# Kernel optimization log

Measured on AMD Instinct MI355X. Metric: run time of the kernel, lower is better.

## Reference

```python
import jax, jax.numpy as jnp
import numpy as np

D_MODEL = 1024
N_Q = 16
N_KV = 4
GRP = N_Q // N_KV
DQ = 64
DV = 64
B = 2
S = 2048
EPS = 1e-5


def _rope(x):
    # x: (N, S, ..., d) with sequence on axis 1; interleaved-pair rotary, theta=10000
    seq, d = x.shape[1], x.shape[-1]
    inv_freq = 1.0 / (10000.0 ** (jnp.arange(0, d, 2, dtype=jnp.float32) / d))
    ang = jnp.arange(seq, dtype=jnp.float32)[:, None] * inv_freq[None, :]  # (S, d/2)
    bshape = (1, seq) + (1,) * (x.ndim - 3) + (d // 2,)
    cos = jnp.cos(ang).reshape(bshape).astype(x.dtype)
    sin = jnp.sin(ang).reshape(bshape).astype(x.dtype)
    x1, x2 = x[..., 0::2], x[..., 1::2]
    r1 = x1 * cos - x2 * sin
    r2 = x1 * sin + x2 * cos
    return jnp.stack([r1, r2], axis=-1).reshape(x.shape)


def _layer_norm(x, gamma, beta):
    mu = jnp.mean(x, axis=-1, keepdims=True)
    var = jnp.var(x, axis=-1, keepdims=True)
    return (x - mu) * jax.lax.rsqrt(var + EPS) * gamma + beta


def setup_inputs() -> dict:
    key = jax.random.key(0)
    ks = jax.random.split(key, 13)
    scale = 0.02
    return {
        "query_sequences": jax.random.normal(ks[0], (B, S, D_MODEL), jnp.float32),
        "key_sequences": jax.random.normal(ks[1], (B, S, D_MODEL), jnp.float32),
        "value_sequences": jax.random.normal(ks[2], (B, S, D_MODEL), jnp.float32),
        "key_value_sequence_lengths": jax.random.randint(ks[3], (B,), S // 2, S + 1),
        "ln_gamma": jnp.ones((D_MODEL,), jnp.float32),
        "ln_beta": jnp.zeros((D_MODEL,), jnp.float32),
        "Wq": jax.random.normal(ks[4], (D_MODEL, N_Q * DQ), jnp.float32) * scale,
        "bq": jnp.zeros((N_Q * DQ,), jnp.float32),
        "Wk": jax.random.normal(ks[5], (D_MODEL, N_KV * DQ), jnp.float32) * scale,
        "bk": jnp.zeros((N_KV * DQ,), jnp.float32),
        "Wv": jax.random.normal(ks[6], (D_MODEL, N_KV * DV), jnp.float32) * scale,
        "bv": jnp.zeros((N_KV * DV,), jnp.float32),
        "Wo": jax.random.normal(ks[7], (N_Q * DV, D_MODEL), jnp.float32) * scale,
        "bo": jnp.zeros((D_MODEL,), jnp.float32),
    }


def reference(query_sequences, key_sequences, value_sequences,
              key_value_sequence_lengths, ln_gamma, ln_beta,
              Wq, bq, Wk, bk, Wv, bv, Wo, bo):
    N, t = query_sequences.shape[0], query_sequences.shape[1]
    T = key_sequences.shape[1]
    # pre-LN (self-attn: applied to q, k, v inputs)
    q_in = _layer_norm(query_sequences, ln_gamma, ln_beta)
    k_in = _layer_norm(key_sequences, ln_gamma, ln_beta)
    v_in = _layer_norm(value_sequences, ln_gamma, ln_beta)
    q = (q_in @ Wq + bq).reshape(N, t, N_KV, GRP, DQ)      # (N,t,h,H,d)
    k = (k_in @ Wk + bk).reshape(N, T, N_KV, DQ)           # (N,T,h,d)
    v = (v_in @ Wv + bv).reshape(N, T, N_KV, DV)           # (N,T,h,d)
    q = _rope(q)
    k = _rope(k)
    scores = jnp.einsum('nthHd,nThd->nhHtT', q, k) / jnp.sqrt(jnp.float32(DQ))
    key_pos = jnp.arange(T)
    pad_ok = (key_pos[None, :] < key_value_sequence_lengths[:, None])  # (N,T)
    causal_ok = (jnp.arange(t)[:, None] >= key_pos[None, :])           # (t,T)
    mask = pad_ok[:, None, None, None, :] & causal_ok[None, None, None, :, :]
    scores = jnp.where(mask, scores, -jnp.inf)
    attn = jax.nn.softmax(scores, axis=-1)                 # (N,h,H,t,T)
    attn_viz = jnp.transpose(attn, (0, 2, 1, 3, 4))        # (N,H,h,t,T)
    seq = jnp.einsum('nhHtT,nThd->nthHd', attn, v).reshape(N, t, N_Q * DV)
    out = seq @ Wo + bo
    return out, attn_viz
```

## Files before the change

### kernel.cpp

```cpp
#include <hip/hip_runtime.h>
#include <hip/hip_bf16.h>

#define S_LEN 2048
#define DM 1024

typedef __attribute__((ext_vector_type(8))) short s16x8;
typedef __attribute__((ext_vector_type(4))) float f32x4;
typedef __attribute__((ext_vector_type(4))) ushort u16x4;

__device__ __forceinline__ ushort f2bf(float f){
  union { float f; unsigned u; } v; v.f = f;
  unsigned r = (v.u + 0x7FFFu + ((v.u >> 16) & 1u)) >> 16;
  return (ushort)r;
}

__device__ __forceinline__ f32x4 mfma16(s16x8 a, s16x8 b, f32x4 c){
  return __builtin_amdgcn_mfma_f32_16x16x32_bf16(a, b, c, 0, 0, 0);
}

__device__ __forceinline__ void gl_lds16(const ushort* g, ushort* l){
  __builtin_amdgcn_global_load_lds(
      (const __attribute__((address_space(1))) unsigned int*)g,
      (__attribute__((address_space(3))) unsigned int*)l, 16, 0, 0);
}

__global__ __launch_bounds__(256) void trig_kernel(float* __restrict__ tab){
  int idx = blockIdx.x*256 + threadIdx.x;
  int t = idx >> 5, i2 = idx & 31;
  float inv = exp2f(-(float)i2 * 0.4152410118609203f);
  float ang = (float)t * inv;
  tab[2*idx]   = cosf(ang);
  tab[2*idx+1] = sinf(ang);
}

__global__ __launch_bounds__(256) void ln_kernel(const float* __restrict__ x,
    const float* __restrict__ g, const float* __restrict__ be, ushort* __restrict__ o){
  int row = blockIdx.x;
  int tid = threadIdx.x;
  const float* xr = x + (size_t)row*DM;
  float4 xv = *(const float4*)(xr + tid*4);
  float s  = xv.x+xv.y+xv.z+xv.w;
  float s2 = xv.x*xv.x+xv.y*xv.y+xv.z*xv.z+xv.w*xv.w;
  for (int m=1;m<64;m<<=1){ s += __shfl_xor(s,m); s2 += __shfl_xor(s2,m); }
  __shared__ float red[8];
  int w = tid>>6, l = tid&63;
  if (l==0){ red[w]=s; red[4+w]=s2; }
  __syncthreads();
  float ts = red[0]+red[1]+red[2]+red[3];
  float t2 = red[4]+red[5]+red[6]+red[7];
  float mu  = ts*(1.0f/DM);
  float var = t2*(1.0f/DM) - mu*mu;
  float rs  = rsqrtf(var + 1e-5f);
  float vals[4] = {xv.x,xv.y,xv.z,xv.w};
  const float* gp = g + tid*4;
  const float* bp = be + tid*4;
  u16x4 ov;
  #pragma unroll
  for (int j=0;j<4;j++) ov[j] = f2bf((vals[j]-mu)*rs*gp[j] + bp[j]);
  *(u16x4*)(o + (size_t)row*DM + tid*4) = ov;
}

__global__ __launch_bounds__(256) void wtr_kernel(const float* __restrict__ in,
    ushort* __restrict__ out, int N){
  __shared__ float lsf[32][36];
  int tid = threadIdx.x;
  int n0 = blockIdx.x*32, k0 = blockIdx.y*32;
  int kr = tid>>3, nc = (tid&7)*4;
  float4 v = *(const float4*)(in + (size_t)(k0+kr)*N + n0 + nc);
  *(float4*)&lsf[kr][nc] = v;
  __syncthreads();
  int nr = tid>>3, kc = (tid&7)*4;
  u16x4 o;
  #pragma unroll
  for (int j=0;j<4;j++) o[j] = f2bf(lsf[kc+j][nr]);
  *(u16x4*)(out + (size_t)(n0+nr)*DM + k0 + kc) = o;
}

__global__ __launch_bounds__(256) void utr_kernel(const ushort* __restrict__ vb,
    ushort* __restrict__ vt){
  __shared__ ushort lst[64*72];
  int tid = threadIdx.x;
  int t0 = blockIdx.x*64;
  int y = blockIdx.y; int n = y>>2, h = y&3;
  int Tr = tid>>2, dg = (tid&3)*16;
  const ushort* ip = vb + ((size_t)(n*S_LEN + t0 + Tr))*256 + h*64 + dg;
  *(s16x8*)&lst[Tr*72 + dg]     = *(const s16x8*)ip;
  *(s16x8*)&lst[Tr*72 + dg + 8] = *(const s16x8*)(ip+8);
  __syncthreads();
  int d = tid>>2, Tg = (tid&3)*16;
  ushort* op = vt + ((size_t)(y*64 + d))*S_LEN + t0 + Tg;
  #pragma unroll
  for (int q=0;q<4;q++){
    u16x4 o;
    #pragma unroll
    for (int j=0;j<4;j++) o[j] = lst[(Tg+4*q+j)*72 + d];
    *(u16x4*)(op + 4*q) = o;
  }
}

template<int BN, bool ROPE, bool F32OUT>
__global__ __launch_bounds__(256) void gemm_kernel(
    const ushort* __restrict__ A, const ushort* __restrict__ BT,
    const float* __restrict__ bias, const float* __restrict__ tab,
    void* __restrict__ Cv, int N, int K){
  constexpr int NB = BN/32;
  __shared__ ushort Als[128*32];
  __shared__ ushort Bls[BN*32];
  int tid = threadIdx.x;
  int w = tid>>6, l = tid&63, lg = l>>4, li = l&15;
  int wr = w>>1, wc = w&1;
  int mbase = blockIdx.y*128, nbase = blockIdx.x*BN;
  f32x4 acc[4][NB];
  #pragma unroll
  for (int m=0;m<4;m++)
    #pragma unroll
    for (int n=0;n<NB;n++) acc[m][n] = (f32x4){0.f,0.f,0.f,0.f};
  int cr = l>>2, ck = (l&3)*8;
  for (int kk=0; kk<K; kk+=32){
    __syncthreads();
    #pragma unroll
    for (int s=0;s<2;s++){
      int ch = w*2+s;
      gl_lds16(A + (size_t)(mbase + ch*16 + cr)*K + kk + ck, &Als[ch*512]);
    }
    #pragma unroll
    for (int s=0;s<BN/64;s++){
      int ch = w*(BN/64)+s;
      gl_lds16(BT + (size_t)(nbase + ch*16 + cr)*K + kk + ck, &Bls[ch*512]);
    }
    __syncthreads();
    s16x8 af[4], bf[NB];
    #pragma unroll
    for (int m=0;m<4;m++) af[m] = *(const s16x8*)&Als[(wr*64 + m*16 + li)*32 + lg*8];
    #pragma unroll
    for (int n=0;n<NB;n++) bf[n] = *(const s16x8*)&Bls[(wc*(BN/2) + n*16 + li)*32 + lg*8];
    #pragma unroll
    for (int m=0;m<4;m++)
      #pragma unroll
      for (int n=0;n<NB;n++)
        acc[m][n] = mfma16(af[m], bf[n], acc[m][n]);
  }
  #pragma unroll
  for (int n=0;n<NB;n++){
    int gcol = nbase + wc*(BN/2) + n*16 + li;
    float bv = bias[gcol];
    #pragma unroll
    for (int m=0;m<4;m++){
      #pragma unroll
      for (int r=0;r<4;r++){
        int grow = mbase + wr*64 + m*16 + 4*lg + r;
        float val = acc[m][n][r] + bv;
        if (ROPE){
          int t = grow & (S_LEN-1);
          int d = gcol & 63;
          const float* tp = tab + t*64 + (d & 62);
          float cv = tp[0], sv = tp[1];
          float other = __shfl_xor(val, 1);
          val = (d & 1) ? (other*sv + val*cv) : (val*cv - other*sv);
        }
        if (F32OUT) ((float*)Cv)[(size_t)grow*N + gcol] = val;
        else        ((ushort*)Cv)[(size_t)grow*N + gcol] = f2bf(val);
      }
    }
  }
}

__global__ __launch_bounds__(256) void flash_kernel(
    const ushort* __restrict__ qg, const ushort* __restrict__ kg,
    const ushort* __restrict__ vt, const int* __restrict__ lens,
    ushort* __restrict__ seq, float* __restrict__ mbuf, float* __restrict__ lbuf){
  __shared__ ushort kls[64*72];
  __shared__ ushort vls[64*72];
  __shared__ ushort pls[64*72];
  int tid = threadIdx.x;
  int w = tid>>6, l = tid&63, lg = l>>4, li = l&15;
  int qbase = blockIdx.x*64;
  int qh = blockIdx.y;
  int n  = blockIdx.z;
  int h = qh>>2;
  int len = lens[n];
  const float L2E = 1.4426950408889634f;

  int trow = qbase + 16*w + li;
  const ushort* qp = qg + ((size_t)n*S_LEN + trow)*1024 + qh*64 + 8*lg;
  s16x8 qf0 = *(const s16x8*)qp;
  s16x8 qf1 = *(const s16x8*)(qp + 32);

  int sT = tid>>2, sdg = (tid&3)*16;
  const ushort* kp = kg + ((size_t)n*S_LEN + sT)*256 + h*64 + sdg;
  const ushort* vp = vt + ((size_t)((n*4+h)*64 + sT))*S_LEN + sdg;

  float m_r[4], l_r[4];
  f32x4 oacc[4];
  #pragma unroll
  for (int r=0;r<4;r++){ m_r[r] = -1e30f; l_r[r] = 0.f; }
  #pragma unroll
  for (int c=0;c<4;c++) oacc[c] = (f32x4){0.f,0.f,0.f,0.f};
  int Tlim = min(qbase + 63, len - 1);
  int nComp = (Tlim >> 6) + 1;

  for (int it=0; it<nComp; ++it){
    int Tb = it*64;
    __syncthreads();
    { const ushort* kpp = kp + (size_t)Tb*256;
      *(s16x8*)&kls[sT*72 + sdg]     = *(const s16x8*)kpp;
      *(s16x8*)&kls[sT*72 + sdg + 8] = *(const s16x8*)(kpp + 8);
      const ushort* vpp = vp + Tb;
      *(s16x8*)&vls[sT*72 + sdg]     = *(const s16x8*)vpp;
      *(s16x8*)&vls[sT*72 + sdg + 8] = *(const s16x8*)(vpp + 8);
    }
    __syncthreads();
    f32x4 sc[4];
    #pragma unroll
    for (int c=0;c<4;c++) sc[c] = (f32x4){0.f,0.f,0.f,0.f};
    #pragma unroll
    for (int c=0;c<4;c++){
      s16x8 b0 = *(const s16x8*)&kls[(16*c+li)*72 + 8*lg];
      s16x8 b1 = *(const s16x8*)&kls[(16*c+li)*72 + 8*lg + 32];
      sc[c] = mfma16(qf0, b0, sc[c]);
      sc[c] = mfma16(qf1, b1, sc[c]);
    }
    #pragma unroll
    for (int c=0;c<4;c++){
      int Tg = Tb + 16*c + li;
      bool colp = Tg < len;
      #pragma unroll
      for (int r=0;r<4;r++){
        int tg = qbase + 16*w + 4*lg + r;
        sc[c][r] = (colp && Tg <= tg) ? sc[c][r]*0.125f : -1e30f;
      }
    }
    float sf[4];
    #pragma unroll
    for (int r=0;r<4;r++){
      float tmax = fmaxf(fmaxf(sc[0][r], sc[1][r]), fmaxf(sc[2][r], sc[3][r]));
      for (int msk=1; msk<16; msk<<=1) tmax = fmaxf(tmax, __shfl_xor(tmax, msk));
      float mn = fmaxf(m_r[r], tmax);
      #pragma unroll
      for (int c=0;c<4;c++) sc[c][r] = exp2f((sc[c][r]-mn)*L2E);
      float ssum = sc[0][r]+sc[1][r]+sc[2][r]+sc[3][r];
      for (int msk=1; msk<16; msk<<=1) ssum += __shfl_xor(ssum, msk);
      sf[r] = exp2f((m_r[r]-mn)*L2E);
      l_r[r] = l_r[r]*sf[r] + ssum;
      m_r[r] = mn;
    }
    #pragma unroll
    for (int c=0;c<4;c++)
      #pragma unroll
      for (int r=0;r<4;r++) oacc[c][r] *= sf[r];
    #pragma unroll
    for (int c=0;c<4;c++)
      #pragma unroll
      for (int r=0;r<4;r++)
        pls[(16*w + 4*lg + r)*72 + 16*c + li] = f2bf(sc[c][r]);
    #pragma unroll
    for (int f=0; f<2; f++){
      s16x8 pa = *(const s16x8*)&pls[(16*w + li)*72 + 8*lg + 32*f];
      #pragma unroll
      for (int c=0;c<4;c++){
        s16x8 vf = *(const s16x8*)&vls[(16*c+li)*72 + 8*lg + 32*f];
        oacc[c] = mfma16(pa, vf, oacc[c]);
      }
    }
  }

  float inv_l[4];
  #pragma unroll
  for (int r=0;r<4;r++) inv_l[r] = 1.0f / l_r[r];
  #pragma unroll
  for (int c=0;c<4;c++){
    #pragma unroll
    for (int r=0;r<4;r++){
      int tg = qbase + 16*w + 4*lg + r;
      seq[((size_t)n*S_LEN + tg)*1024 + qh*64 + 16*c + li] = f2bf(oacc[c][r]*inv_l[r]);
    }
  }
  int zi = n*16 + qh;
  if (li == 0){
    #pragma unroll
    for (int r=0;r<4;r++){
      int tg = qbase + 16*w + 4*lg + r;
      mbuf[(size_t)zi*S_LEN + tg] = m_r[r];
      lbuf[(size_t)zi*S_LEN + tg] = inv_l[r];
    }
  }
}

__global__ __launch_bounds__(256) void viz_kernel(
    const ushort* __restrict__ qg, const ushort* __restrict__ kg,
    const int* __restrict__ lens, const float* __restrict__ mbuf,
    const float* __restrict__ lbuf, float* __restrict__ viz){
  __shared__ ushort kls[64*72];
  __shared__ float pfs[64*72];
  int tid = threadIdx.x;
  int Tb = blockIdx.x*64;
  int qbase = blockIdx.y*64;
  int zi = blockIdx.z;
  int n = zi>>4, qh = zi&15;
  int h = qh>>2, H = qh&3;
  int len = lens[n];
  float* vizp = viz + (size_t)((n*4 + H)*4 + h) * S_LEN * S_LEN;

  if (Tb > qbase + 63 || Tb >= len){
    int row = qbase + (tid>>2);
    float* zp = vizp + (size_t)row*S_LEN + Tb + (tid&3)*16;
    f32x4 zv = (f32x4){0.f,0.f,0.f,0.f};
    #pragma unroll
    for (int u=0;u<4;u++) *(f32x4*)(zp + 4*u) = zv;
    return;
  }

  int w = tid>>6, l = tid&63, lg = l>>4, li = l&15;
  const float L2E = 1.4426950408889634f;
  int trow = qbase + 16*w + li;
  const ushort* qp = qg + ((size_t)n*S_LEN + trow)*1024 + qh*64 + 8*lg;
  s16x8 qf0 = *(const s16x8*)qp;
  s16x8 qf1 = *(const s16x8*)(qp + 32);
  int sT = tid>>2, sdg = (tid&3)*16;
  const ushort* kpp = kg + ((size_t)n*S_LEN + Tb + sT)*256 + h*64 + sdg;
  *(s16x8*)&kls[sT*72 + sdg]     = *(const s16x8*)kpp;
  *(s16x8*)&kls[sT*72 + sdg + 8] = *(const s16x8*)(kpp + 8);

  float m_r[4], il_r[4];
  #pragma unroll
  for (int r=0;r<4;r++){
    int tg = qbase + 16*w + 4*lg + r;
    m_r[r]  = mbuf[(size_t)zi*S_LEN + tg];
    il_r[r] = lbuf[(size_t)zi*S_LEN + tg];
  }
  __syncthreads();

  f32x4 sc[4];
  #pragma unroll
  for (int c=0;c<4;c++) sc[c] = (f32x4){0.f,0.f,0.f,0.f};
  #pragma unroll
  for (int c=0;c<4;c++){
    s16x8 b0 = *(const s16x8*)&kls[(16*c+li)*72 + 8*lg];
    s16x8 b1 = *(const s16x8*)&kls[(16*c+li)*72 + 8*lg + 32];
    sc[c] = mfma16(qf0, b0, sc[c]);
    sc[c] = mfma16(qf1, b1, sc[c]);
  }
  #pragma unroll
  for (int c=0;c<4;c++){
    int Tg = Tb + 16*c + li;
    bool colp = Tg < len;
    #pragma unroll
    for (int r=0;r<4;r++){
      int tg = qbase + 16*w + 4*lg + r;
      bool ok = colp && (Tg <= tg);
      float p = exp2f((sc[c][r]*0.125f - m_r[r])*L2E) * il_r[r];
      pfs[(16*w + 4*lg + r)*72 + 16*c + li] = ok ? p : 0.f;
    }
  }
  __syncthreads();
  int row = tid>>2, c4 = (tid&3)*4;
  float* op = vizp + (size_t)(qbase+row)*S_LEN + Tb + c4;
  #pragma unroll
  for (int u=0;u<4;u++)
    *(f32x4*)(op + 16*u) = *(f32x4*)&pfs[row*72 + c4 + 16*u];
}

extern "C" void kernel_launch(void* const* d_in, const int* in_sizes, int n_in,
                              void* d_out, int out_size, void* d_ws, size_t ws_size,
                              hipStream_t stream){
  const float* xq = (const float*)d_in[0];
  const float* xk = (const float*)d_in[1];
  const float* xv = (const float*)d_in[2];
  const int*  lens= (const int*)d_in[3];
  const float* g  = (const float*)d_in[4];
  const float* be = (const float*)d_in[5];
  const float* Wq = (const float*)d_in[6];
  const float* bq = (const float*)d_in[7];
  const float* Wk = (const float*)d_in[8];
  const float* bk = (const float*)d_in[9];
  const float* Wv = (const float*)d_in[10];
  const float* bv = (const float*)d_in[11];
  const float* Wo = (const float*)d_in[12];
  const float* bo = (const float*)d_in[13];

  ushort* ws  = (ushort*)d_ws;
  ushort* xnq = ws;
  ushort* xnk = ws + 4194304;
  ushort* xnv = ws + 8388608;
  ushort* qb  = ws + 12582912;
  ushort* kb  = ws + 16777216;
  ushort* vb  = ws + 17825792;
  ushort* vt  = ws + 18874368;
  ushort* WqT = ws + 19922944;
  ushort* WkT = ws + 20971520;
  ushort* WvT = ws + 21233664;
  ushort* WoT = ws + 21495808;
  float*  tab = (float*)(ws + 22544384);
  float*  mbuf= (float*)(ws + 22806528);
  float*  lbuf= (float*)(ws + 22937600);
  ushort* seqb = xnq;

  float* outp = (float*)d_out;
  float* vizp = outp + (size_t)4194304;

  trig_kernel<<<256,256,0,stream>>>(tab);
  ln_kernel<<<4096,256,0,stream>>>(xq, g, be, xnq);
  ln_kernel<<<4096,256,0,stream>>>(xk, g, be, xnk);
  ln_kernel<<<4096,256,0,stream>>>(xv, g, be, xnv);
  wtr_kernel<<<dim3(32,32),256,0,stream>>>(Wq, WqT, 1024);
  wtr_kernel<<<dim3( 8,32),256,0,stream>>>(Wk, WkT, 256);
  wtr_kernel<<<dim3( 8,32),256,0,stream>>>(Wv, WvT, 256);
  wtr_kernel<<<dim3(32,32),256,0,stream>>>(Wo, WoT, 1024);
  gemm_kernel<128,true ,false><<<dim3(8,32),256,0,stream>>>(xnq, WqT, bq, tab, qb, 1024, 1024);
  gemm_kernel< 64,true ,false><<<dim3(4,32),256,0,stream>>>(xnk, WkT, bk, tab, kb,  256, 1024);
  gemm_kernel< 64,false,false><<<dim3(4,32),256,0,stream>>>(xnv, WvT, bv, tab, vb,  256, 1024);
  utr_kernel<<<dim3(32,8),256,0,stream>>>(vb, vt);
  flash_kernel<<<dim3(32,16,2),256,0,stream>>>(qb, kb, vt, lens, seqb, mbuf, lbuf);
  viz_kernel<<<dim3(32,32,32),256,0,stream>>>(qb, kb, lens, mbuf, lbuf, vizp);
  gemm_kernel<128,false,true ><<<dim3(8,32),256,0,stream>>>(seqb, WoT, bo, tab, (void*)outp, 1024, 1024);
}
```

Measured before the change: 866.3 us.

## Merge K/V projections, retile GEMMs, widen flash key blocks, batch viz tiles

```diff
diff --git a/kernel.cpp b/kernel.cpp
--- a/kernel.cpp
+++ b/kernel.cpp
@@ -33,11 +33,13 @@
   tab[2*idx+1] = sinf(ang);
 }
 
-__global__ __launch_bounds__(256) void ln_kernel(const float* __restrict__ x,
+__global__ __launch_bounds__(256) void ln3_kernel(const float* __restrict__ x0,
+    const float* __restrict__ x1, const float* __restrict__ x2,
     const float* __restrict__ g, const float* __restrict__ be, ushort* __restrict__ o){
   int row = blockIdx.x;
   int tid = threadIdx.x;
-  const float* xr = x + (size_t)row*DM;
+  const float* xs = (blockIdx.y==0) ? x0 : (blockIdx.y==1) ? x1 : x2;
+  const float* xr = xs + (size_t)row*DM;
   float4 xv = *(const float4*)(xr + tid*4);
   float s  = xv.x+xv.y+xv.z+xv.w;
   float s2 = xv.x*xv.x+xv.y*xv.y+xv.z*xv.z+xv.w*xv.w;
@@ -57,7 +59,7 @@
   u16x4 ov;
   #pragma unroll
   for (int j=0;j<4;j++) ov[j] = f2bf((vals[j]-mu)*rs*gp[j] + bp[j]);
-  *(u16x4*)(o + (size_t)row*DM + tid*4) = ov;
+  *(u16x4*)(o + (size_t)blockIdx.y*4194304 + (size_t)row*DM + tid*4) = ov;
 }
 
 __global__ __launch_bounds__(256) void wtr_kernel(const float* __restrict__ in,
@@ -76,14 +78,14 @@
   *(u16x4*)(out + (size_t)(n0+nr)*DM + k0 + kc) = o;
 }
 
-__global__ __launch_bounds__(256) void utr_kernel(const ushort* __restrict__ vb,
+__global__ __launch_bounds__(256) void utr_kernel(const ushort* __restrict__ kvb,
     ushort* __restrict__ vt){
   __shared__ ushort lst[64*72];
   int tid = threadIdx.x;
   int t0 = blockIdx.x*64;
   int y = blockIdx.y; int n = y>>2, h = y&3;
   int Tr = tid>>2, dg = (tid&3)*16;
-  const ushort* ip = vb + ((size_t)(n*S_LEN + t0 + Tr))*256 + h*64 + dg;
+  const ushort* ip = kvb + ((size_t)(n*S_LEN + t0 + Tr))*512 + 256 + h*64 + dg;
   *(s16x8*)&lst[Tr*72 + dg]     = *(const s16x8*)ip;
   *(s16x8*)&lst[Tr*72 + dg + 8] = *(const s16x8*)(ip+8);
   __syncthreads();
@@ -98,59 +100,74 @@
   }
 }
 
-template<int BN, bool ROPE, bool F32OUT>
+template<int BM, int MODE>
 __global__ __launch_bounds__(256) void gemm_kernel(
-    const ushort* __restrict__ A, const ushort* __restrict__ BT,
-    const float* __restrict__ bias, const float* __restrict__ tab,
+    const ushort* __restrict__ A, const ushort* __restrict__ A2,
+    const ushort* __restrict__ BT, const float* __restrict__ bias,
+    const float* __restrict__ bias2, const float* __restrict__ tab,
     void* __restrict__ Cv, int N, int K){
-  constexpr int NB = BN/32;
-  __shared__ ushort Als[128*32];
-  __shared__ ushort Bls[BN*32];
+  constexpr int MF = 2;
+  constexpr int NF = (BM == 128) ? 4 : 2;
+  constexpr int ACALLS = BM/32;
+  __shared__ ushort Als[BM*64];
+  __shared__ ushort Bls[64*64];
   int tid = threadIdx.x;
   int w = tid>>6, l = tid&63, lg = l>>4, li = l&15;
-  int wr = w>>1, wc = w&1;
-  int mbase = blockIdx.y*128, nbase = blockIdx.x*BN;
-  f32x4 acc[4][NB];
-  #pragma unroll
-  for (int m=0;m<4;m++)
-    #pragma unroll
-    for (int n=0;n<NB;n++) acc[m][n] = (f32x4){0.f,0.f,0.f,0.f};
-  int cr = l>>2, ck = (l&3)*8;
-  for (int kk=0; kk<K; kk+=32){
-    __syncthreads();
+  int wrow = (BM==128) ? w*32 : (w>>1)*32;
+  int wcol = (BM==128) ? 0 : (w&1)*32;
+  int mbase = blockIdx.y*BM, nbase = blockIdx.x*64;
+  const ushort* Ause = A;
+  if (MODE==2 && nbase >= 256) Ause = A2;
+  f32x4 acc[MF][NF];
+  #pragma unroll
+  for (int m=0;m<MF;m++)
+    #pragma unroll
+    for (int n=0;n<NF;n++) acc[m][n] = (f32x4){0.f,0.f,0.f,0.f};
+  for (int kk=0; kk<K; kk+=64){
+    __syncthreads();
+    #pragma unroll
+    for (int s=0;s<ACALLS;s++){
+      int idx = s*256 + tid;
+      int row = idx>>3, ch = idx&7;
+      gl_lds16(Ause + (size_t)(mbase+row)*K + kk + 8*(ch ^ (row&7)),
+               &Als[(size_t)(s*256 + w*64)*8]);
+    }
     #pragma unroll
     for (int s=0;s<2;s++){
-      int ch = w*2+s;
-      gl_lds16(A + (size_t)(mbase + ch*16 + cr)*K + kk + ck, &Als[ch*512]);
-    }
-    #pragma unroll
-    for (int s=0;s<BN/64;s++){
-      int ch = w*(BN/64)+s;
-      gl_lds16(BT + (size_t)(nbase + ch*16 + cr)*K + kk + ck, &Bls[ch*512]);
-    }
-    __syncthreads();
-    s16x8 af[4], bf[NB];
-    #pragma unroll
-    for (int m=0;m<4;m++) af[m] = *(const s16x8*)&Als[(wr*64 + m*16 + li)*32 + lg*8];
-    #pragma unroll
-    for (int n=0;n<NB;n++) bf[n] = *(const s16x8*)&Bls[(wc*(BN/2) + n*16 + li)*32 + lg*8];
-    #pragma unroll
-    for (int m=0;m<4;m++)
-      #pragma unroll
-      for (int n=0;n<NB;n++)
-        acc[m][n] = mfma16(af[m], bf[n], acc[m][n]);
-  }
-  #pragma unroll
-  for (int n=0;n<NB;n++){
-    int gcol = nbase + wc*(BN/2) + n*16 + li;
-    float bv = bias[gcol];
-    #pragma unroll
-    for (int m=0;m<4;m++){
+      int idx = s*256 + tid;
+      int row = idx>>3, ch = idx&7;
+      gl_lds16(BT + (size_t)(nbase+row)*K + kk + 8*(ch ^ (row&7)),
+               &Bls[(size_t)(s*256 + w*64)*8]);
+    }
+    __syncthreads();
+    #pragma unroll
+    for (int f=0;f<2;f++){
+      s16x8 af[MF], bfv[NF];
+      #pragma unroll
+      for (int m=0;m<MF;m++)
+        af[m] = *(const s16x8*)&Als[(wrow+m*16+li)*64 + 8*((lg+4*f) ^ (li&7))];
+      #pragma unroll
+      for (int n=0;n<NF;n++)
+        bfv[n] = *(const s16x8*)&Bls[(wcol+n*16+li)*64 + 8*((lg+4*f) ^ (li&7))];
+      #pragma unroll
+      for (int m=0;m<MF;m++)
+        #pragma unroll
+        for (int n=0;n<NF;n++)
+          acc[m][n] = mfma16(af[m], bfv[n], acc[m][n]);
+    }
+  }
+  bool doRope = (MODE==1) || (MODE==2 && nbase < 256);
+  #pragma unroll
+  for (int n=0;n<NF;n++){
+    int gcol = nbase + wcol + n*16 + li;
+    float bv0 = (MODE==2 && nbase>=256) ? bias2[gcol-256] : bias[gcol];
+    #pragma unroll
+    for (int m=0;m<MF;m++){
       #pragma unroll
       for (int r=0;r<4;r++){
-        int grow = mbase + wr*64 + m*16 + 4*lg + r;
-        float val = acc[m][n][r] + bv;
-        if (ROPE){
+        int grow = mbase + wrow + m*16 + 4*lg + r;
+        float val = acc[m][n][r] + bv0;
+        if (doRope){
           int t = grow & (S_LEN-1);
           int d = gcol & 63;
           const float* tp = tab + t*64 + (d & 62);
@@ -158,20 +175,20 @@
           float other = __shfl_xor(val, 1);
           val = (d & 1) ? (other*sv + val*cv) : (val*cv - other*sv);
         }
-        if (F32OUT) ((float*)Cv)[(size_t)grow*N + gcol] = val;
-        else        ((ushort*)Cv)[(size_t)grow*N + gcol] = f2bf(val);
+        if (MODE==3) ((float*)Cv)[(size_t)grow*N + gcol] = val;
+        else         ((ushort*)Cv)[(size_t)grow*N + gcol] = f2bf(val);
       }
     }
   }
 }
 
 __global__ __launch_bounds__(256) void flash_kernel(
-    const ushort* __restrict__ qg, const ushort* __restrict__ kg,
+    const ushort* __restrict__ qg, const ushort* __restrict__ kvb,
     const ushort* __restrict__ vt, const int* __restrict__ lens,
     ushort* __restrict__ seq, float* __restrict__ mbuf, float* __restrict__ lbuf){
-  __shared__ ushort kls[64*72];
-  __shared__ ushort vls[64*72];
-  __shared__ ushort pls[64*72];
+  __shared__ ushort kls[128*72];
+  __shared__ ushort vls[64*136];
+  __shared__ ushort pls[64*136];
   int tid = threadIdx.x;
   int w = tid>>6, l = tid&63, lg = l>>4, li = l&15;
   int qbase = blockIdx.x*64;
@@ -186,9 +203,10 @@
   s16x8 qf0 = *(const s16x8*)qp;
   s16x8 qf1 = *(const s16x8*)(qp + 32);
 
-  int sT = tid>>2, sdg = (tid&3)*16;
-  const ushort* kp = kg + ((size_t)n*S_LEN + sT)*256 + h*64 + sdg;
-  const ushort* vp = vt + ((size_t)((n*4+h)*64 + sT))*S_LEN + sdg;
+  int sT2 = tid>>1, sd2 = (tid&1)*32;
+  int dv  = tid>>2, tc  = (tid&3)*32;
+  const ushort* kp = kvb + ((size_t)n*S_LEN + sT2)*512 + h*64 + sd2;
+  const ushort* vp = vt + ((size_t)((n*4+h)*64 + dv))*S_LEN + tc;
 
   float m_r[4], l_r[4];
   f32x4 oacc[4];
@@ -197,31 +215,35 @@
   #pragma unroll
   for (int c=0;c<4;c++) oacc[c] = (f32x4){0.f,0.f,0.f,0.f};
   int Tlim = min(qbase + 63, len - 1);
-  int nComp = (Tlim >> 6) + 1;
-
-  for (int it=0; it<nComp; ++it){
-    int Tb = it*64;
-    __syncthreads();
-    { const ushort* kpp = kp + (size_t)Tb*256;
-      *(s16x8*)&kls[sT*72 + sdg]     = *(const s16x8*)kpp;
-      *(s16x8*)&kls[sT*72 + sdg + 8] = *(const s16x8*)(kpp + 8);
+  int nR = (Tlim >> 7) + 1;
+
+  for (int it=0; it<nR; ++it){
+    int Tb = it*128;
+    __syncthreads();
+    { const ushort* kpp = kp + (size_t)Tb*512;
+      #pragma unroll
+      for (int j=0;j<4;j++)
+        *(s16x8*)&kls[sT2*72 + sd2 + 8*j] = *(const s16x8*)(kpp + 8*j);
       const ushort* vpp = vp + Tb;
-      *(s16x8*)&vls[sT*72 + sdg]     = *(const s16x8*)vpp;
-      *(s16x8*)&vls[sT*72 + sdg + 8] = *(const s16x8*)(vpp + 8);
-    }
-    __syncthreads();
-    f32x4 sc[4];
-    #pragma unroll
-    for (int c=0;c<4;c++) sc[c] = (f32x4){0.f,0.f,0.f,0.f};
-    #pragma unroll
-    for (int c=0;c<4;c++){
+      #pragma unroll
+      for (int j=0;j<4;j++)
+        *(s16x8*)&vls[dv*136 + tc + 8*j] = *(const s16x8*)(vpp + 8*j);
+    }
+    __syncthreads();
+    f32x4 sc[8];
+    #pragma unroll
+    for (int c=0;c<8;c++) sc[c] = (f32x4){0.f,0.f,0.f,0.f};
+    __builtin_amdgcn_s_setprio(1);
+    #pragma unroll
+    for (int c=0;c<8;c++){
       s16x8 b0 = *(const s16x8*)&kls[(16*c+li)*72 + 8*lg];
       s16x8 b1 = *(const s16x8*)&kls[(16*c+li)*72 + 8*lg + 32];
       sc[c] = mfma16(qf0, b0, sc[c]);
       sc[c] = mfma16(qf1, b1, sc[c]);
     }
-    #pragma unroll
-    for (int c=0;c<4;c++){
+    __builtin_amdgcn_s_setprio(0);
+    #pragma unroll
+    for (int c=0;c<8;c++){
       int Tg = Tb + 16*c + li;
       bool colp = Tg < len;
       #pragma unroll
@@ -233,12 +255,14 @@
     float sf[4];
     #pragma unroll
     for (int r=0;r<4;r++){
-      float tmax = fmaxf(fmaxf(sc[0][r], sc[1][r]), fmaxf(sc[2][r], sc[3][r]));
+      float tmax = sc[0][r];
+      #pragma unroll
+      for (int c=1;c<8;c++) tmax = fmaxf(tmax, sc[c][r]);
       for (int msk=1; msk<16; msk<<=1) tmax = fmaxf(tmax, __shfl_xor(tmax, msk));
       float mn = fmaxf(m_r[r], tmax);
-      #pragma unroll
-      for (int c=0;c<4;c++) sc[c][r] = exp2f((sc[c][r]-mn)*L2E);
-      float ssum = sc[0][r]+sc[1][r]+sc[2][r]+sc[3][r];
+      float ssum = 0.f;
+      #pragma unroll
+      for (int c=0;c<8;c++){ sc[c][r] = exp2f((sc[c][r]-mn)*L2E); ssum += sc[c][r]; }
       for (int msk=1; msk<16; msk<<=1) ssum += __shfl_xor(ssum, msk);
       sf[r] = exp2f((m_r[r]-mn)*L2E);
       l_r[r] = l_r[r]*sf[r] + ssum;
@@ -249,19 +273,21 @@
       #pragma unroll
       for (int r=0;r<4;r++) oacc[c][r] *= sf[r];
     #pragma unroll
-    for (int c=0;c<4;c++)
+    for (int c=0;c<8;c++)
       #pragma unroll
       for (int r=0;r<4;r++)
-        pls[(16*w + 4*lg + r)*72 + 16*c + li] = f2bf(sc[c][r]);
-    #pragma unroll
-    for (int f=0; f<2; f++){
-      s16x8 pa = *(const s16x8*)&pls[(16*w + li)*72 + 8*lg + 32*f];
+        pls[(16*w + 4*lg + r)*136 + 16*c + li] = f2bf(sc[c][r]);
+    __builtin_amdgcn_s_setprio(1);
+    #pragma unroll
+    for (int f=0; f<4; f++){
+      s16x8 pa = *(const s16x8*)&pls[(16*w + li)*136 + 8*lg + 32*f];
       #pragma unroll
       for (int c=0;c<4;c++){
-        s16x8 vf = *(const s16x8*)&vls[(16*c+li)*72 + 8*lg + 32*f];
+        s16x8 vf = *(const s16x8*)&vls[(16*c+li)*136 + 8*lg + 32*f];
         oacc[c] = mfma16(pa, vf, oacc[c]);
       }
     }
+    __builtin_amdgcn_s_setprio(0);
   }
 
   float inv_l[4];
@@ -287,77 +313,78 @@
 }
 
 __global__ __launch_bounds__(256) void viz_kernel(
-    const ushort* __restrict__ qg, const ushort* __restrict__ kg,
+    const ushort* __restrict__ qg, const ushort* __restrict__ kvb,
     const int* __restrict__ lens, const float* __restrict__ mbuf,
     const float* __restrict__ lbuf, float* __restrict__ viz){
   __shared__ ushort kls[64*72];
-  __shared__ float pfs[64*72];
-  int tid = threadIdx.x;
-  int Tb = blockIdx.x*64;
+  int tid = threadIdx.x;
+  int Tb0 = blockIdx.x*256;
   int qbase = blockIdx.y*64;
   int zi = blockIdx.z;
   int n = zi>>4, qh = zi&15;
   int h = qh>>2, H = qh&3;
   int len = lens[n];
   float* vizp = viz + (size_t)((n*4 + H)*4 + h) * S_LEN * S_LEN;
-
-  if (Tb > qbase + 63 || Tb >= len){
-    int row = qbase + (tid>>2);
-    float* zp = vizp + (size_t)row*S_LEN + Tb + (tid&3)*16;
-    f32x4 zv = (f32x4){0.f,0.f,0.f,0.f};
-    #pragma unroll
-    for (int u=0;u<4;u++) *(f32x4*)(zp + 4*u) = zv;
-    return;
-  }
-
   int w = tid>>6, l = tid&63, lg = l>>4, li = l&15;
   const float L2E = 1.4426950408889634f;
-  int trow = qbase + 16*w + li;
-  const ushort* qp = qg + ((size_t)n*S_LEN + trow)*1024 + qh*64 + 8*lg;
-  s16x8 qf0 = *(const s16x8*)qp;
-  s16x8 qf1 = *(const s16x8*)(qp + 32);
-  int sT = tid>>2, sdg = (tid&3)*16;
-  const ushort* kpp = kg + ((size_t)n*S_LEN + Tb + sT)*256 + h*64 + sdg;
-  *(s16x8*)&kls[sT*72 + sdg]     = *(const s16x8*)kpp;
-  *(s16x8*)&kls[sT*72 + sdg + 8] = *(const s16x8*)(kpp + 8);
-
+
+  bool anyComp = (Tb0 <= qbase + 63) && (Tb0 < len);
+  s16x8 qf0, qf1;
   float m_r[4], il_r[4];
-  #pragma unroll
-  for (int r=0;r<4;r++){
-    int tg = qbase + 16*w + 4*lg + r;
-    m_r[r]  = mbuf[(size_t)zi*S_LEN + tg];
-    il_r[r] = lbuf[(size_t)zi*S_LEN + tg];
-  }
-  __syncthreads();
-
-  f32x4 sc[4];
-  #pragma unroll
-  for (int c=0;c<4;c++) sc[c] = (f32x4){0.f,0.f,0.f,0.f};
-  #pragma unroll
-  for (int c=0;c<4;c++){
-    s16x8 b0 = *(const s16x8*)&kls[(16*c+li)*72 + 8*lg];
-    s16x8 b1 = *(const s16x8*)&kls[(16*c+li)*72 + 8*lg + 32];
-    sc[c] = mfma16(qf0, b0, sc[c]);
-    sc[c] = mfma16(qf1, b1, sc[c]);
-  }
-  #pragma unroll
-  for (int c=0;c<4;c++){
-    int Tg = Tb + 16*c + li;
-    bool colp = Tg < len;
+  if (anyComp){
+    int trow = qbase + 16*w + li;
+    const ushort* qp = qg + ((size_t)n*S_LEN + trow)*1024 + qh*64 + 8*lg;
+    qf0 = *(const s16x8*)qp;
+    qf1 = *(const s16x8*)(qp + 32);
     #pragma unroll
     for (int r=0;r<4;r++){
       int tg = qbase + 16*w + 4*lg + r;
-      bool ok = colp && (Tg <= tg);
-      float p = exp2f((sc[c][r]*0.125f - m_r[r])*L2E) * il_r[r];
-      pfs[(16*w + 4*lg + r)*72 + 16*c + li] = ok ? p : 0.f;
-    }
-  }
-  __syncthreads();
-  int row = tid>>2, c4 = (tid&3)*4;
-  float* op = vizp + (size_t)(qbase+row)*S_LEN + Tb + c4;
-  #pragma unroll
-  for (int u=0;u<4;u++)
-    *(f32x4*)(op + 16*u) = *(f32x4*)&pfs[row*72 + c4 + 16*u];
+      m_r[r]  = mbuf[(size_t)zi*S_LEN + tg];
+      il_r[r] = lbuf[(size_t)zi*S_LEN + tg];
+    }
+  }
+
+  int sT = tid>>2, sdg = (tid&3)*16;
+  for (int s=0; s<4; ++s){
+    int Tb = Tb0 + s*64;
+    bool zero = (Tb > qbase + 63) || (Tb >= len);
+    if (zero){
+      int row = qbase + (tid>>2);
+      float* zp = vizp + (size_t)row*S_LEN + Tb + (tid&3)*16;
+      f32x4 zv = (f32x4){0.f,0.f,0.f,0.f};
+      #pragma unroll
+      for (int u=0;u<4;u++) *(f32x4*)(zp + 4*u) = zv;
+      continue;
+    }
+    __syncthreads();
+    { const ushort* kpp = kvb + ((size_t)n*S_LEN + Tb + sT)*512 + h*64 + sdg;
+      *(s16x8*)&kls[sT*72 + sdg]     = *(const s16x8*)kpp;
+      *(s16x8*)&kls[sT*72 + sdg + 8] = *(const s16x8*)(kpp + 8);
+    }
+    __syncthreads();
+    f32x4 sc[4];
+    #pragma unroll
+    for (int c=0;c<4;c++) sc[c] = (f32x4){0.f,0.f,0.f,0.f};
+    #pragma unroll
+    for (int c=0;c<4;c++){
+      s16x8 b0 = *(const s16x8*)&kls[(16*c+li)*72 + 8*lg];
+      s16x8 b1 = *(const s16x8*)&kls[(16*c+li)*72 + 8*lg + 32];
+      sc[c] = mfma16(qf0, b0, sc[c]);
+      sc[c] = mfma16(qf1, b1, sc[c]);
+    }
+    #pragma unroll
+    for (int c=0;c<4;c++){
+      int Tg = Tb + 16*c + li;
+      bool colp = Tg < len;
+      #pragma unroll
+      for (int r=0;r<4;r++){
+        int tg = qbase + 16*w + 4*lg + r;
+        bool ok = colp && (Tg <= tg);
+        float p = ok ? exp2f((sc[c][r]*0.125f - m_r[r])*L2E) * il_r[r] : 0.f;
+        vizp[(size_t)tg*S_LEN + Tg] = p;
+      }
+    }
+  }
 }
 
 extern "C" void kernel_launch(void* const* d_in, const int* in_sizes, int n_in,
@@ -383,12 +410,10 @@
   ushort* xnk = ws + 4194304;
   ushort* xnv = ws + 8388608;
   ushort* qb  = ws + 12582912;
-  ushort* kb  = ws + 16777216;
-  ushort* vb  = ws + 17825792;
+  ushort* kvb = ws + 16777216;
   ushort* vt  = ws + 18874368;
   ushort* WqT = ws + 19922944;
-  ushort* WkT = ws + 20971520;
-  ushort* WvT = ws + 21233664;
+  ushort* WkvT= ws + 20971520;
   ushort* WoT = ws + 21495808;
   float*  tab = (float*)(ws + 22544384);
   float*  mbuf= (float*)(ws + 22806528);
@@ -399,18 +424,15 @@
   float* vizp = outp + (size_t)4194304;
 
   trig_kernel<<<256,256,0,stream>>>(tab);
-  ln_kernel<<<4096,256,0,stream>>>(xq, g, be, xnq);
-  ln_kernel<<<4096,256,0,stream>>>(xk, g, be, xnk);
-  ln_kernel<<<4096,256,0,stream>>>(xv, g, be, xnv);
+  ln3_kernel<<<dim3(4096,3),256,0,stream>>>(xq, xk, xv, g, be, xnq);
   wtr_kernel<<<dim3(32,32),256,0,stream>>>(Wq, WqT, 1024);
-  wtr_kernel<<<dim3( 8,32),256,0,stream>>>(Wk, WkT, 256);
-  wtr_kernel<<<dim3( 8,32),256,0,stream>>>(Wv, WvT, 256);
+  wtr_kernel<<<dim3( 8,32),256,0,stream>>>(Wk, WkvT, 256);
+  wtr_kernel<<<dim3( 8,32),256,0,stream>>>(Wv, WkvT + (size_t)256*1024, 256);
   wtr_kernel<<<dim3(32,32),256,0,stream>>>(Wo, WoT, 1024);
-  gemm_kernel<128,true ,false><<<dim3(8,32),256,0,stream>>>(xnq, WqT, bq, tab, qb, 1024, 1024);
-  gemm_kernel< 64,true ,false><<<dim3(4,32),256,0,stream>>>(xnk, WkT, bk, tab, kb,  256, 1024);
-  gemm_kernel< 64,false,false><<<dim3(4,32),256,0,stream>>>(xnv, WvT, bv, tab, vb,  256, 1024);
-  utr_kernel<<<dim3(32,8),256,0,stream>>>(vb, vt);
-  flash_kernel<<<dim3(32,16,2),256,0,stream>>>(qb, kb, vt, lens, seqb, mbuf, lbuf);
-  viz_kernel<<<dim3(32,32,32),256,0,stream>>>(qb, kb, lens, mbuf, lbuf, vizp);
-  gemm_kernel<128,false,true ><<<dim3(8,32),256,0,stream>>>(seqb, WoT, bo, tab, (void*)outp, 1024, 1024);
-}
+  gemm_kernel<128,1><<<dim3(16,32),256,0,stream>>>(xnq, nullptr, WqT, bq, nullptr, tab, qb, 1024, 1024);
+  gemm_kernel< 64,2><<<dim3( 8,64),256,0,stream>>>(xnk, xnv, WkvT, bk, bv, tab, kvb, 512, 1024);
+  utr_kernel<<<dim3(32,8),256,0,stream>>>(kvb, vt);
+  flash_kernel<<<dim3(32,16,2),256,0,stream>>>(qb, kvb, vt, lens, seqb, mbuf, lbuf);
+  viz_kernel<<<dim3(8,32,32),256,0,stream>>>(qb, kvb, lens, mbuf, lbuf, vizp);
+  gemm_kernel<128,3><<<dim3(16,32),256,0,stream>>>(seqb, nullptr, WoT, bo, nullptr, tab, (void*)outp, 1024, 1024);
+}
```

Result: faster. 847.5 us (-2.2%).
